# Optimization experiments

Hardware: AMD Instinct MI355X
Metric: run time of the kernel (lower is better)

The kernel has to match this reference:

```python
import jax, jax.numpy as jnp
import numpy as np

N, E, D, K, H = 100000, 1600000, 32, 3, 1


def setup_inputs() -> dict:
    key = jax.random.key(0)
    ks = jax.random.split(key, 7)
    return {
        "src": jax.random.randint(ks[0], (E,), 0, N),
        "dst": jax.random.randint(ks[1], (E,), 0, N),
        "embedding": jax.random.normal(ks[2], (N, D), jnp.float32),
        "lambda_max": jnp.full((1,), 2.0, jnp.float32),
        # ChebConv: single Linear(k*d -> d) over concatenated Chebyshev terms (shared by both calls)
        "cheb_W": jax.random.normal(ks[3], (K * D, D), jnp.float32) / np.sqrt(K * D),
        "cheb_b": jnp.zeros((D,), jnp.float32),
        # GATv2: fc_src / fc_dst Linear(d -> H*d) + attention vector (H, d)
        "gat_W_src": jax.random.normal(ks[4], (D, H * D), jnp.float32) / np.sqrt(D),
        "gat_b_src": jnp.zeros((H * D,), jnp.float32),
        "gat_W_dst": jax.random.normal(ks[5], (D, H * D), jnp.float32) / np.sqrt(D),
        "gat_b_dst": jnp.zeros((H * D,), jnp.float32),
        "gat_attn": jax.random.normal(ks[6], (H, D), jnp.float32) / np.sqrt(D),
    }


def _cheb(src, dst, feat, lam, W, b, n):
    # DGL ChebConv with lambda_max given; activation = leaky_relu (slope 0.01)
    deg = jnp.clip(jax.ops.segment_sum(jnp.ones(src.shape[0], feat.dtype), dst, num_segments=n), 1.0)
    dinv = deg[:, None] ** -0.5  # D^{-1/2}, (N,1)
    re_norm = 2.0 / lam[0]

    def unnL(f):  # D^{-1/2} A D^{-1/2} f
        return jax.ops.segment_sum((f * dinv)[src], dst, num_segments=n) * dinv

    X0 = feat
    X1 = -re_norm * unnL(X0) + X0 * (re_norm - 1.0)
    Xs = [X0, X1]
    for _ in range(2, K):
        Xi = -2.0 * re_norm * unnL(X1) + X1 * (2.0 * (re_norm - 1.0)) - X0
        Xs.append(Xi)
        X0, X1 = X1, Xi
    return jax.nn.leaky_relu(jnp.concatenate(Xs, axis=1) @ W + b, 0.01)


def _gatv2(src, dst, h, Ws, bs, Wd, bd, attn, n):
    Hh, Dd = attn.shape
    fs = (h @ Ws + bs).reshape(n, Hh, Dd)  # feat_src 'el'
    fd = (h @ Wd + bd).reshape(n, Hh, Dd)  # feat_dst 'er'
    e = jax.nn.leaky_relu(fs[src] + fd[dst], 0.2)        # (E,H,D), GATv2 negative_slope=0.2
    logits = jnp.einsum('ehd,hd->eh', e, attn)           # (E,H)
    m = jax.ops.segment_max(logits, dst, num_segments=n)  # per-dst softmax (edge_softmax)
    ex = jnp.exp(logits - m[dst])
    a = ex / jax.ops.segment_sum(ex, dst, num_segments=n)[dst]
    ft = jax.ops.segment_sum(fs[src] * a[..., None], dst, num_segments=n)  # (N,H,D)
    return jax.nn.leaky_relu(ft, 0.01)  # activation=F.leaky_relu


def reference(src, dst, embedding, lambda_max, cheb_W, cheb_b,
              gat_W_src, gat_b_src, gat_W_dst, gat_b_dst, gat_attn):
    n, d = embedding.shape
    h = _cheb(src, dst, embedding, lambda_max, cheb_W, cheb_b, n)
    h = _cheb(src, dst, h, lambda_max, cheb_W, cheb_b, n)
    out = _gatv2(src, dst, h, gat_W_src, gat_b_src, gat_W_dst, gat_b_dst, gat_attn, n)
    return out.reshape(-1, d)
```

## Files before the change

### kernel.cpp

```cpp
#include <hip/hip_runtime.h>

#define TPB 256
#define TPB2 512
#define NB 512
#define CAPB 4096
#define CHUNK 4096

__global__ void k_zero_u(unsigned int* p, int n){
  int i = blockIdx.x*TPB + threadIdx.x;
  if(i < n) p[i] = 0u;
}

__global__ __launch_bounds__(TPB2) void k_bin1(const int* __restrict__ src,
    const int* __restrict__ dst,
    unsigned int* __restrict__ btail, unsigned int* __restrict__ binned,
    int E, int npb){
  __shared__ unsigned int hist[NB];
  __shared__ unsigned int lofs[NB];
  __shared__ unsigned int base[NB];
  __shared__ unsigned int s[TPB2];
  __shared__ int2 stage[CHUNK];
  int t = threadIdx.x;
  hist[t] = 0u;
  __syncthreads();
  int e0 = blockIdx.x*CHUNK;
  int e1 = e0 + CHUNK; if(e1 > E) e1 = E;
  for(int e = e0 + t; e < e1; e += TPB2)
    atomicAdd(&hist[dst[e]/npb], 1u);
  __syncthreads();
  unsigned int a0 = hist[t];
  s[t] = a0; __syncthreads();
  for(int off = 1; off < TPB2; off <<= 1){
    unsigned int x = (t >= off) ? s[t - off] : 0u;
    __syncthreads();
    s[t] += x;
    __syncthreads();
  }
  unsigned int excl = s[t] - a0;
  lofs[t] = excl;
  base[t] = a0 ? atomicAdd(btail + t, a0) : 0u;
  __syncthreads();
  hist[t] = excl;
  __syncthreads();
  for(int e = e0 + t; e < e1; e += TPB2){
    int d = dst[e];
    int b = d / npb;
    unsigned int p = atomicAdd(&hist[b], 1u);
    stage[p] = make_int2(src[e], d);
  }
  __syncthreads();
  int tot = e1 - e0;
  for(int i = t; i < tot; i += TPB2){
    int2 sd = stage[i];
    int b = sd.y / npb;
    unsigned int go = base[b] + ((unsigned)i - lofs[b]);
    if(go < (unsigned)CAPB)
      binned[(size_t)b*CAPB + go] = ((unsigned)sd.x << 8) | (unsigned)(sd.y - b*npb);
  }
}

__global__ __launch_bounds__(TPB) void k_scanb(const unsigned int* __restrict__ btail,
    unsigned int* __restrict__ bbase, unsigned int* __restrict__ ptr, int N, int E){
  __shared__ unsigned int s[TPB];
  __shared__ unsigned int carry;
  int t = threadIdx.x;
  if(t == 0) carry = 0u;
  __syncthreads();
  for(int base = 0; base < NB; base += TPB){
    unsigned int v = btail[base + t];
    s[t] = v; __syncthreads();
    for(int off = 1; off < TPB; off <<= 1){
      unsigned int x = (t >= off) ? s[t - off] : 0u;
      __syncthreads();
      s[t] += x;
      __syncthreads();
    }
    bbase[base + t] = s[t] - v + carry;
    __syncthreads();
    if(t == 0) carry += s[TPB-1];
    __syncthreads();
  }
  if(t == 0) ptr[N] = (unsigned int)E;
}

__global__ __launch_bounds__(TPB) void k_bin2x(const unsigned int* __restrict__ binned,
    const unsigned int* __restrict__ btail, const unsigned int* __restrict__ bbase,
    unsigned int* __restrict__ ptr, float* __restrict__ dinv,
    int* __restrict__ csr, int npb, int N){
  __shared__ unsigned int ebuf[CAPB];
  __shared__ int obuf[CAPB];
  __shared__ unsigned int cnt_s[256];
  __shared__ unsigned int s[TPB];
  __shared__ unsigned int curs[256];
  int b = blockIdx.x;
  int n0 = b*npb; if(n0 >= N) return;
  int t = threadIdx.x;
  unsigned int cnt = btail[b]; if(cnt > (unsigned)CAPB) cnt = CAPB;
  unsigned int segbase = bbase[b];
  cnt_s[t] = 0u;
  __syncthreads();
  for(unsigned int i = t; i < cnt; i += TPB){
    unsigned int e = binned[(size_t)b*CAPB + i];
    ebuf[i] = e;
    atomicAdd(&cnt_s[e & 255u], 1u);
  }
  __syncthreads();
  unsigned int v = cnt_s[t];
  s[t] = v; __syncthreads();
  for(int off = 1; off < TPB; off <<= 1){
    unsigned int x = (t >= off) ? s[t - off] : 0u;
    __syncthreads();
    s[t] += x;
    __syncthreads();
  }
  unsigned int lo = s[t] - v;
  int n = n0 + t;
  if(t < npb && n < N){
    ptr[n]  = segbase + lo;
    dinv[n] = 1.0f / sqrtf(fmaxf((float)v, 1.0f));
  }
  curs[t] = lo;
  __syncthreads();
  for(unsigned int i = t; i < cnt; i += TPB){
    unsigned int e = ebuf[i];
    unsigned int p = atomicAdd(&curs[e & 255u], 1u);
    obuf[p] = (int)(e >> 8);
  }
  __syncthreads();
  for(unsigned int i = t; i < cnt; i += TPB)
    csr[segbase + i] = obuf[i];
}

__device__ __forceinline__ float4 agg_gather4(const unsigned int* __restrict__ ptr,
    const int* __restrict__ csr,
    const float* __restrict__ X, const float* __restrict__ dinv, int t, int lane){
  int g  = lane >> 3;
  int f4 = (lane & 7) << 2;
  unsigned int p0 = ptr[t], p1 = ptr[t+1];
  float4 S0 = make_float4(0.f,0.f,0.f,0.f);
  float4 S1 = make_float4(0.f,0.f,0.f,0.f);
  for(unsigned int base = p0; base < p1; base += 32){
    int idx = 0; float dva = 0.f;
    unsigned int pos = base + (unsigned)lane;
    if(pos < p1){ idx = csr[pos]; dva = dinv[idx]; }
    unsigned int cnt = p1 - base; if(cnt > 32u) cnt = 32u;
    unsigned int rounds = (cnt + 3u) >> 2;
    for(unsigned int r = 0; r < rounds; r += 2){
      int el0 = (int)(r << 2) + g;
      int s0  = __shfl(idx, el0, 32);
      float d0 = __shfl(dva, el0, 32);
      const float4 x0 = *(const float4*)(X + (size_t)s0*32 + f4);
      if(r + 1 < rounds){
        int el1 = el0 + 4;
        int s1  = __shfl(idx, el1, 32);
        float d1 = __shfl(dva, el1, 32);
        const float4 x1 = *(const float4*)(X + (size_t)s1*32 + f4);
        S1.x += x1.x*d1; S1.y += x1.y*d1; S1.z += x1.z*d1; S1.w += x1.w*d1;
      }
      S0.x += x0.x*d0; S0.y += x0.y*d0; S0.z += x0.z*d0; S0.w += x0.w*d0;
    }
  }
  float4 S;
  S.x = S0.x + S1.x; S.y = S0.y + S1.y; S.z = S0.z + S1.z; S.w = S0.w + S1.w;
  S.x += __shfl_xor(S.x, 8, 32);  S.y += __shfl_xor(S.y, 8, 32);
  S.z += __shfl_xor(S.z, 8, 32);  S.w += __shfl_xor(S.w, 8, 32);
  S.x += __shfl_xor(S.x, 16, 32); S.y += __shfl_xor(S.y, 16, 32);
  S.z += __shfl_xor(S.z, 16, 32); S.w += __shfl_xor(S.w, 16, 32);
  return S;
}

__global__ __launch_bounds__(TPB) void k_cheb1(const unsigned int* __restrict__ ptr,
    const int* __restrict__ csr,
    const float* __restrict__ X0, const float* __restrict__ dinv,
    const float* __restrict__ lam, float* __restrict__ X1, int N){
  int t = blockIdx.x*8 + (threadIdx.x >> 5);
  if(t >= N) return;
  int lane = threadIdx.x & 31;
  float4 S = agg_gather4(ptr, csr, X0, dinv, t, lane);
  if((lane >> 3) != 0) return;
  int f4 = (lane & 7) << 2;
  float re = 2.0f / lam[0];
  float dt = dinv[t];
  size_t o = (size_t)t*32 + f4;
  const float4 x0 = *(const float4*)(X0 + o);
  float4 r;
  r.x = -re*(S.x*dt) + (re-1.0f)*x0.x;
  r.y = -re*(S.y*dt) + (re-1.0f)*x0.y;
  r.z = -re*(S.z*dt) + (re-1.0f)*x0.z;
  r.w = -re*(S.w*dt) + (re-1.0f)*x0.w;
  *(float4*)(X1 + o) = r;
}

__global__ __launch_bounds__(TPB) void k_cheb2(const unsigned int* __restrict__ ptr,
    const int* __restrict__ csr,
    const float* __restrict__ X0, const float* __restrict__ X1,
    const float* __restrict__ dinv, const float* __restrict__ lam,
    float* __restrict__ X2, int N){
  int t = blockIdx.x*8 + (threadIdx.x >> 5);
  if(t >= N) return;
  int lane = threadIdx.x & 31;
  float4 S = agg_gather4(ptr, csr, X1, dinv, t, lane);
  if((lane >> 3) != 0) return;
  int f4 = (lane & 7) << 2;
  float re = 2.0f / lam[0];
  float dt = dinv[t];
  size_t o = (size_t)t*32 + f4;
  const float4 x0 = *(const float4*)(X0 + o);
  const float4 x1 = *(const float4*)(X1 + o);
  float c1 = -2.0f*re, c2 = 2.0f*(re-1.0f);
  float4 r;
  r.x = c1*(S.x*dt) + c2*x1.x - x0.x;
  r.y = c1*(S.y*dt) + c2*x1.y - x0.y;
  r.z = c1*(S.z*dt) + c2*x1.z - x0.z;
  r.w = c1*(S.w*dt) + c2*x1.w - x0.w;
  *(float4*)(X2 + o) = r;
}

__global__ __launch_bounds__(TPB) void k_lin(const float* __restrict__ X0,
    const float* __restrict__ X1,
    const float* __restrict__ X2, const float* __restrict__ W,
    const float* __restrict__ b, float* __restrict__ out, int N){
  __shared__ float4 Wt4[32*24];
  int tid = threadIdx.x;
  for(int i = tid; i < 32*24; i += TPB){
    int c = i / 24, j = i % 24;
    Wt4[i] = make_float4(W[(size_t)(4*j+0)*32 + c], W[(size_t)(4*j+1)*32 + c],
                         W[(size_t)(4*j+2)*32 + c], W[(size_t)(4*j+3)*32 + c]);
  }
  __syncthreads();
  int n = blockIdx.x*TPB + tid;
  if(n >= N) return;
  float acc[32];
  #pragma unroll
  for(int c = 0; c < 32; c++) acc[c] = b[c];
  const float* xs0 = X0 + (size_t)n*32;
  const float* xs1 = X1 + (size_t)n*32;
  const float* xs2 = X2 + (size_t)n*32;
  #pragma unroll
  for(int s3 = 0; s3 < 3; s3++){
    const float4* xp = (const float4*)(s3 == 0 ? xs0 : (s3 == 1 ? xs1 : xs2));
    #pragma unroll
    for(int q = 0; q < 8; q++){
      float4 xv = xp[q];
      int j = s3*8 + q;
      #pragma unroll
      for(int c = 0; c < 32; c++){
        float4 w4 = Wt4[c*24 + j];
        acc[c] += xv.x*w4.x + xv.y*w4.y + xv.z*w4.z + xv.w*w4.w;
      }
    }
  }
  float4* op = (float4*)(out + (size_t)n*32);
  #pragma unroll
  for(int q = 0; q < 8; q++){
    float4 v;
    float a;
    a = acc[4*q+0]; v.x = a > 0.f ? a : 0.01f*a;
    a = acc[4*q+1]; v.y = a > 0.f ? a : 0.01f*a;
    a = acc[4*q+2]; v.z = a > 0.f ? a : 0.01f*a;
    a = acc[4*q+3]; v.w = a > 0.f ? a : 0.01f*a;
    op[q] = v;
  }
}

__global__ __launch_bounds__(TPB) void k_fc(const float* __restrict__ h,
    const float* __restrict__ Wsr, const float* __restrict__ bsr,
    const float* __restrict__ Wds, const float* __restrict__ bds,
    float* __restrict__ fs, float* __restrict__ fd, int N){
  int n = blockIdx.x*TPB + threadIdx.x;
  if(n >= N) return;
  float as[32], ad[32];
  #pragma unroll
  for(int c = 0; c < 32; c++){ as[c] = bsr[c]; ad[c] = bds[c]; }
  const float4* xp = (const float4*)(h + (size_t)n*32);
  #pragma unroll
  for(int q = 0; q < 8; q++){
    float4 xv = xp[q];
    const float* Wr = Wsr + (size_t)(q*4)*32;
    const float* Vr = Wds + (size_t)(q*4)*32;
    #pragma unroll
    for(int c = 0; c < 32; c++){
      as[c] += xv.x*Wr[c] + xv.y*Wr[32+c] + xv.z*Wr[64+c] + xv.w*Wr[96+c];
      ad[c] += xv.x*Vr[c] + xv.y*Vr[32+c] + xv.z*Vr[64+c] + xv.w*Vr[96+c];
    }
  }
  float4* sp = (float4*)(fs + (size_t)n*32);
  float4* dp = (float4*)(fd + (size_t)n*32);
  #pragma unroll
  for(int q = 0; q < 8; q++){
    float4 v1, v2;
    v1.x = as[4*q+0]; v1.y = as[4*q+1]; v1.z = as[4*q+2]; v1.w = as[4*q+3];
    v2.x = ad[4*q+0]; v2.y = ad[4*q+1]; v2.z = ad[4*q+2]; v2.w = ad[4*q+3];
    sp[q] = v1;
    dp[q] = v2;
  }
}

__global__ __launch_bounds__(TPB) void k_gat(const unsigned int* __restrict__ ptr,
    const int* __restrict__ csr,
    const float* __restrict__ fs, const float* __restrict__ fd,
    const float* __restrict__ attn, float* __restrict__ out, int N){
  int t = blockIdx.x*8 + (threadIdx.x >> 5);
  if(t >= N) return;
  int lane = threadIdx.x & 31;
  int g  = lane >> 3;
  int f4 = (lane & 7) << 2;
  unsigned int p0 = ptr[t], p1 = ptr[t+1];
  const float4 fd4 = *(const float4*)(fd + (size_t)t*32 + f4);
  const float4 at4 = *(const float4*)(attn + f4);
  float m = -3.402823466e38f, den = 0.f;
  float4 acc = make_float4(0.f,0.f,0.f,0.f);
  for(unsigned int base = p0; base < p1; base += 32){
    int idx = 0;
    unsigned int pos = base + (unsigned)lane;
    if(pos < p1) idx = csr[pos];
    unsigned int cnt = p1 - base; if(cnt > 32u) cnt = 32u;
    unsigned int rounds = (cnt + 3u) >> 2;
    for(unsigned int r = 0; r < rounds; r++){
      int el = (int)(r << 2) + g;
      int s  = __shfl(idx, el, 32);
      const float4 f = *(const float4*)(fs + (size_t)s*32 + f4);
      float vx = f.x + fd4.x; vx = vx > 0.f ? vx : 0.2f*vx;
      float vy = f.y + fd4.y; vy = vy > 0.f ? vy : 0.2f*vy;
      float vz = f.z + fd4.z; vz = vz > 0.f ? vz : 0.2f*vz;
      float vw = f.w + fd4.w; vw = vw > 0.f ? vw : 0.2f*vw;
      float pl = vx*at4.x + vy*at4.y + vz*at4.z + vw*at4.w;
      pl += __shfl_xor(pl, 4, 32);
      pl += __shfl_xor(pl, 2, 32);
      pl += __shfl_xor(pl, 1, 32);
      if(el < (int)cnt){
        float mn = fmaxf(m, pl);
        float sc = __expf(m - mn);
        float e  = __expf(pl - mn);
        den = den*sc + e;
        acc.x = acc.x*sc + f.x*e;
        acc.y = acc.y*sc + f.y*e;
        acc.z = acc.z*sc + f.z*e;
        acc.w = acc.w*sc + f.w*e;
        m = mn;
      }
    }
  }
  #pragma unroll
  for(int off = 8; off <= 16; off <<= 1){
    float mo = __shfl_xor(m, off, 32);
    float do_ = __shfl_xor(den, off, 32);
    float ax = __shfl_xor(acc.x, off, 32);
    float ay = __shfl_xor(acc.y, off, 32);
    float az = __shfl_xor(acc.z, off, 32);
    float aw = __shfl_xor(acc.w, off, 32);
    float mn = fmaxf(m, mo);
    float a = __expf(m - mn), b = __expf(mo - mn);
    den = den*a + do_*b;
    acc.x = acc.x*a + ax*b;
    acc.y = acc.y*a + ay*b;
    acc.z = acc.z*a + az*b;
    acc.w = acc.w*a + aw*b;
    m = mn;
  }
  if(g != 0) return;
  float4 o = make_float4(0.f,0.f,0.f,0.f);
  if(den > 0.f){
    float inv = 1.0f / den;
    o.x = acc.x*inv; o.x = o.x > 0.f ? o.x : 0.01f*o.x;
    o.y = acc.y*inv; o.y = o.y > 0.f ? o.y : 0.01f*o.y;
    o.z = acc.z*inv; o.z = o.z > 0.f ? o.z : 0.01f*o.z;
    o.w = acc.w*inv; o.w = o.w > 0.f ? o.w : 0.01f*o.w;
  }
  *(float4*)(out + (size_t)t*32 + f4) = o;
}

extern "C" void kernel_launch(void* const* d_in, const int* in_sizes, int n_in,
                              void* d_out, int out_size, void* d_ws, size_t ws_size,
                              hipStream_t stream){
  const int*   src = (const int*)d_in[0];
  const int*   dst = (const int*)d_in[1];
  const float* emb = (const float*)d_in[2];
  const float* lam = (const float*)d_in[3];
  const float* cW  = (const float*)d_in[4];
  const float* cB  = (const float*)d_in[5];
  const float* gWs = (const float*)d_in[6];
  const float* gbs = (const float*)d_in[7];
  const float* gWd = (const float*)d_in[8];
  const float* gbd = (const float*)d_in[9];
  const float* gat = (const float*)d_in[10];
  const int E  = in_sizes[0];
  const int N  = in_sizes[2] / 32;
  const int NF = N * 32;
  const int npb = (N + NB - 1) / NB;

  int gN  = (N + TPB-1)/TPB;
  int gR  = (N + 7)/8;
  int gB1 = (E + CHUNK-1)/CHUNK;

  char* p = (char*)d_ws;
  auto alloc = [&](size_t bytes)->char*{ char* r = p; p += (bytes + 255) & ~(size_t)255; return r; };
  unsigned int* ptrA = (unsigned int*)alloc((size_t)(N+1)*4);
  unsigned int* btail= (unsigned int*)alloc((size_t)NB*4);
  unsigned int* bbase= (unsigned int*)alloc((size_t)NB*4);
  float* dinv = (float*)alloc((size_t)N*4);
  int*   csr  = (int*)alloc((size_t)E*4);
  float* X1   = (float*)alloc((size_t)NF*4);
  float* X2   = (float*)alloc((size_t)NF*4);
  float* h1   = (float*)alloc((size_t)NF*4);
  float* h2   = (float*)alloc((size_t)NF*4);
  unsigned int* binned = (unsigned int*)X1;

  k_zero_u<<<(NB+TPB-1)/TPB, TPB, 0, stream>>>(btail, NB);
  k_bin1<<<gB1, TPB2, 0, stream>>>(src, dst, btail, binned, E, npb);
  k_scanb<<<1, TPB, 0, stream>>>(btail, bbase, ptrA, N, E);
  k_bin2x<<<NB, TPB, 0, stream>>>(binned, btail, bbase, ptrA, dinv, csr, npb, N);

  k_cheb1<<<gR, TPB, 0, stream>>>(ptrA, csr, emb, dinv, lam, X1, N);
  k_cheb2<<<gR, TPB, 0, stream>>>(ptrA, csr, emb, X1, dinv, lam, X2, N);
  k_lin<<<gN, TPB, 0, stream>>>(emb, X1, X2, cW, cB, h1, N);

  k_cheb1<<<gR, TPB, 0, stream>>>(ptrA, csr, h1, dinv, lam, X1, N);
  k_cheb2<<<gR, TPB, 0, stream>>>(ptrA, csr, h1, X1, dinv, lam, X2, N);
  k_lin<<<gN, TPB, 0, stream>>>(h1, X1, X2, cW, cB, h2, N);

  k_fc<<<gN, TPB, 0, stream>>>(h2, gWs, gbs, gWd, gbd, X1 , X2 , N);
  k_gat<<<gR, TPB, 0, stream>>>(ptrA, csr, X1, X2, gat, (float*)d_out, N);
}
```

Baseline: 392.3 us.

## Fuse second Chebyshev step with the linear projection into one kernel

Merges k_cheb2 and k_lin into k_cheb2l. Each warp computes X2 for its node, stages X0, X1 and X2 in shared memory, and each lane then computes one output column against a padded, transposed copy of W held in shared memory. This removes the X2 global write and the re-reads of X0, X1 and X2 by a separate kernel, and drops two launches. In exchange, every block now loads the full weight matrix into shared memory, and the matvec runs on the gather kernel's warp-per-node layout, which may cost occupancy.

After: 421.3 us. 1.07x slower.

```diff
diff --git a/kernel.cpp b/kernel.cpp
--- a/kernel.cpp
+++ b/kernel.cpp
@@ -191,17 +191,28 @@
   *(float4*)(X1 + o) = r;
 }
 
-__global__ __launch_bounds__(TPB) void k_cheb2(const unsigned int* __restrict__ ptr,
+__global__ __launch_bounds__(TPB) void k_cheb2l(const unsigned int* __restrict__ ptr,
     const int* __restrict__ csr,
     const float* __restrict__ X0, const float* __restrict__ X1,
     const float* __restrict__ dinv, const float* __restrict__ lam,
-    float* __restrict__ X2, int N){
-  int t = blockIdx.x*8 + (threadIdx.x >> 5);
+    const float* __restrict__ W, const float* __restrict__ b,
+    float* __restrict__ hout, int N){
+  __shared__ float4 Wt[32*25];
+  __shared__ float4 xbuf[8][25];
+  int tid = threadIdx.x;
+  for(int i = tid; i < 32*24; i += TPB){
+    int c = i / 24, j = i % 24;
+    Wt[c*25 + j] = make_float4(W[(size_t)(4*j+0)*32 + c], W[(size_t)(4*j+1)*32 + c],
+                               W[(size_t)(4*j+2)*32 + c], W[(size_t)(4*j+3)*32 + c]);
+  }
+  __syncthreads();
+  int wid  = tid >> 5;
+  int t    = blockIdx.x*8 + wid;
+  int lane = tid & 31;
   if(t >= N) return;
-  int lane = threadIdx.x & 31;
   float4 S = agg_gather4(ptr, csr, X1, dinv, t, lane);
-  if((lane >> 3) != 0) return;
-  int f4 = (lane & 7) << 2;
+  int q  = lane & 7;
+  int f4 = q << 2;
   float re = 2.0f / lam[0];
   float dt = dinv[t];
   size_t o = (size_t)t*32 + f4;
@@ -213,54 +224,20 @@
   r.y = c1*(S.y*dt) + c2*x1.y - x0.y;
   r.z = c1*(S.z*dt) + c2*x1.z - x0.z;
   r.w = c1*(S.w*dt) + c2*x1.w - x0.w;
-  *(float4*)(X2 + o) = r;
-}
-
-__global__ __launch_bounds__(TPB) void k_lin(const float* __restrict__ X0,
-    const float* __restrict__ X1,
-    const float* __restrict__ X2, const float* __restrict__ W,
-    const float* __restrict__ b, float* __restrict__ out, int N){
-  __shared__ float4 Wt4[32*24];
-  int tid = threadIdx.x;
-  for(int i = tid; i < 32*24; i += TPB){
-    int c = i / 24, j = i % 24;
-    Wt4[i] = make_float4(W[(size_t)(4*j+0)*32 + c], W[(size_t)(4*j+1)*32 + c],
-                         W[(size_t)(4*j+2)*32 + c], W[(size_t)(4*j+3)*32 + c]);
-  }
-  __syncthreads();
-  int n = blockIdx.x*TPB + tid;
-  if(n >= N) return;
-  float acc[32];
-  #pragma unroll
-  for(int c = 0; c < 32; c++) acc[c] = b[c];
-  const float* xs0 = X0 + (size_t)n*32;
-  const float* xs1 = X1 + (size_t)n*32;
-  const float* xs2 = X2 + (size_t)n*32;
-  #pragma unroll
-  for(int s3 = 0; s3 < 3; s3++){
-    const float4* xp = (const float4*)(s3 == 0 ? xs0 : (s3 == 1 ? xs1 : xs2));
-    #pragma unroll
-    for(int q = 0; q < 8; q++){
-      float4 xv = xp[q];
-      int j = s3*8 + q;
-      #pragma unroll
-      for(int c = 0; c < 32; c++){
-        float4 w4 = Wt4[c*24 + j];
-        acc[c] += xv.x*w4.x + xv.y*w4.y + xv.z*w4.z + xv.w*w4.w;
-      }
-    }
-  }
-  float4* op = (float4*)(out + (size_t)n*32);
-  #pragma unroll
-  for(int q = 0; q < 8; q++){
-    float4 v;
-    float a;
-    a = acc[4*q+0]; v.x = a > 0.f ? a : 0.01f*a;
-    a = acc[4*q+1]; v.y = a > 0.f ? a : 0.01f*a;
-    a = acc[4*q+2]; v.z = a > 0.f ? a : 0.01f*a;
-    a = acc[4*q+3]; v.w = a > 0.f ? a : 0.01f*a;
-    op[q] = v;
-  }
+  if(lane < 8){
+    xbuf[wid][q]      = x0;
+    xbuf[wid][8 + q]  = x1;
+    xbuf[wid][16 + q] = r;
+  }
+  int c = lane;
+  float acc = b[c];
+  #pragma unroll
+  for(int j = 0; j < 24; j++){
+    float4 w4 = Wt[c*25 + j];
+    float4 x4 = xbuf[wid][j];
+    acc += w4.x*x4.x + w4.y*x4.y + w4.z*x4.z + w4.w*x4.w;
+  }
+  hout[(size_t)t*32 + c] = acc > 0.f ? acc : 0.01f*acc;
 }
 
 __global__ __launch_bounds__(TPB) void k_fc(const float* __restrict__ h,
@@ -412,12 +389,10 @@
   k_bin2x<<<NB, TPB, 0, stream>>>(binned, btail, bbase, ptrA, dinv, csr, npb, N);
 
   k_cheb1<<<gR, TPB, 0, stream>>>(ptrA, csr, emb, dinv, lam, X1, N);
-  k_cheb2<<<gR, TPB, 0, stream>>>(ptrA, csr, emb, X1, dinv, lam, X2, N);
-  k_lin<<<gN, TPB, 0, stream>>>(emb, X1, X2, cW, cB, h1, N);
+  k_cheb2l<<<gR, TPB, 0, stream>>>(ptrA, csr, emb, X1, dinv, lam, cW, cB, h1, N);
 
   k_cheb1<<<gR, TPB, 0, stream>>>(ptrA, csr, h1, dinv, lam, X1, N);
-  k_cheb2<<<gR, TPB, 0, stream>>>(ptrA, csr, h1, X1, dinv, lam, X2, N);
-  k_lin<<<gN, TPB, 0, stream>>>(h1, X1, X2, cW, cB, h2, N);
+  k_cheb2l<<<gR, TPB, 0, stream>>>(ptrA, csr, h1, X1, dinv, lam, cW, cB, h2, N);
 
   k_fc<<<gN, TPB, 0, stream>>>(h2, gWs, gbs, gWd, gbd, X1 , X2 , N);
   k_gat<<<gR, TPB, 0, stream>>>(ptrA, csr, X1, X2, gat, (float*)d_out, N);
```
